# Kernel tuning notes

Measured on AMD Instinct MI355X. Metric: run time of the kernel, lower is better.

## Reference

```python
import jax, jax.numpy as jnp
import numpy as np

N = 4096; E = 65536; IN = 512; H = 256; QD = 256; NH = 8; HD = QD // NH
OUT = 10; L = 2; CT = 50


def _ln(x, g, b, eps=1e-5):
    mu = x.mean(-1, keepdims=True)
    var = ((x - mu) ** 2).mean(-1, keepdims=True)
    return (x - mu) * jax.lax.rsqrt(var + eps) * g + b


def _forward(x, edge_index, cell_types, Wi, bi, Wq, bq, Wk, bk, Wv, bv, Bc, cemb,
             Win, bin_p, Wo, bo, Wm1, bm1, Wm2, bm2, Wm3, bm3, ln_g, ln_b,
             Wc1, bc1, Wc2, bc2):
    src, tgt = edge_index[0], edge_index[1]
    h = jax.nn.relu(x @ Wi + bi)                      # [N, H] input projection
    # graph connectivity scattered into a dense mask (as in _create_attention_mask)
    mask = jnp.zeros((N, N), jnp.float32).at[src, tgt].set(1.0)
    for l in range(L):
        res = h
        Q = h @ Wq[l] + bq[l]                         # [N, QD]
        K = h @ Wk[l] + bk[l]
        V = h @ Wv[l] + bv[l]
        Q = Q @ Bc[l]                                 # biological constraint
        K = K @ Bc[l].T
        ce = cemb[l][cell_types]                      # [N, QD] cell-type embedding
        Q = Q + 0.1 * ce
        K = K + 0.1 * ce
        # dense graph-masked attention (entanglement matrix), applied to V
        scores = (Q @ K.T) / float(np.sqrt(QD))      # [N, N]
        scores = jnp.where(mask == 0.0, -1e9, scores)
        attn = jax.nn.softmax(scores, axis=-1)
        graph_att = attn @ V                          # [N, QD]
        # nn.MultiheadAttention(Q, K, V) entanglement layer (eval mode)
        q = (Q @ Win[l, :, :QD] + bin_p[l, :QD]).reshape(N, NH, HD)
        k = (K @ Win[l, :, QD:2 * QD] + bin_p[l, QD:2 * QD]).reshape(N, NH, HD)
        v = (V @ Win[l, :, 2 * QD:] + bin_p[l, 2 * QD:]).reshape(N, NH, HD)
        w = jax.nn.softmax(jnp.einsum('nhd,mhd->hnm', q, k) / float(np.sqrt(HD)), axis=-1)
        mha = jnp.einsum('hnm,mhd->nhd', w, v).reshape(N, QD) @ Wo[l] + bo[l]
        # edge gather -> message MLP -> scatter-add (PyG aggr='add', x_i=target, x_j=source)
        # quantum slot of the concat is zeros, so only the first 2H rows of Wm1 contribute
        m = jnp.concatenate([h[tgt], h[src]], axis=-1) @ Wm1[l, :2 * H] + bm1[l]
        m = jax.nn.relu(m)
        m = jax.nn.relu(m @ Wm2[l] + bm2[l])
        m = m @ Wm3[l] + bm3[l]                       # [E, H]
        agg = jax.ops.segment_sum(m, tgt, num_segments=N)
        h = _ln(res + agg + mha + graph_att, ln_g[l], ln_b[l])
    # graph-level readout: mean || max pooling -> classifier (hidden*2 -> hidden -> out)
    pooled = jnp.concatenate([h.mean(0), h.max(0)], axis=-1)   # [2H]
    z = jax.nn.relu(pooled @ Wc1 + bc1)
    return z @ Wc2 + bc2                              # [OUT]


def setup_inputs():
    ks = jax.random.split(jax.random.key(0), 40)
    s = 0.05
    p = lambda i, shape: jax.random.normal(ks[i], shape, jnp.float32) * s
    z = lambda shape: jnp.zeros(shape, jnp.float32)
    return {
        'x': jax.random.normal(ks[0], (N, IN), jnp.float32),
        'edge_index': jax.random.randint(ks[1], (2, E), 0, N),
        'cell_types': jax.random.randint(ks[2], (N,), 0, CT),
        'Wi': p(3, (IN, H)), 'bi': z((H,)),
        'Wq': p(4, (L, H, QD)), 'bq': z((L, QD)),
        'Wk': p(5, (L, H, QD)), 'bk': z((L, QD)),
        'Wv': p(6, (L, H, QD)), 'bv': z((L, QD)),
        'Bc': p(7, (L, QD, QD)),
        'cemb': p(8, (L, CT, QD)),
        'Win': p(9, (L, QD, 3 * QD)), 'bin_p': z((L, 3 * QD)),
        'Wo': p(10, (L, QD, QD)), 'bo': z((L, QD)),
        'Wm1': p(11, (L, 2 * H + QD, QD)), 'bm1': z((L, QD)),
        'Wm2': p(12, (L, QD, QD)), 'bm2': z((L, QD)),
        'Wm3': p(13, (L, QD, H)), 'bm3': z((L, H)),
        'ln_g': jnp.ones((L, H), jnp.float32), 'ln_b': z((L, H)),
        'Wc1': p(14, (2 * H, H)), 'bc1': z((H,)),
        'Wc2': p(15, (H, OUT)), 'bc2': z((OUT,)),
    }


def reference(x, edge_index, cell_types, Wi, bi, Wq, bq, Wk, bk, Wv, bv, Bc, cemb,
              Win, bin_p, Wo, bo, Wm1, bm1, Wm2, bm2, Wm3, bm3, ln_g, ln_b,
              Wc1, bc1, Wc2, bc2):
    return _forward(x, edge_index, cell_types, Wi, bi, Wq, bq, Wk, bk, Wv, bv, Bc, cemb,
                    Win, bin_p, Wo, bo, Wm1, bm1, Wm2, bm2, Wm3, bm3, ln_g, ln_b,
                    Wc1, bc1, Wc2, bc2)
```

## Files before the change

### kernel.cpp

```cpp
#include <hip/hip_runtime.h>
#include <hip/hip_bf16.h>

#define N_NODES 4096
#define E_EDGES 65536
#define IN_F    512
#define H_F     256
#define QD      256
#define NHEAD   8
#define HD      32
#define OUT_F   10
#define L_LAYERS 2
#define CT_N    50

enum { FLAG_RELU = 1, FLAG_ACCUM = 2, FLAG_WF32 = 4, FLAG_WB16 = 8 };

typedef __attribute__((ext_vector_type(8))) __bf16 bf16x8;
typedef __attribute__((ext_vector_type(4))) float f32x4;

union PU { bf16x8 v; __hip_bfloat16 h[8]; __hip_bfloat162 b2[4]; };

template<int BM, int BN, bool EDGE>
__global__ __launch_bounds__(256) void gemm_mfma(
    const __hip_bfloat16* __restrict__ A, int lda,
    const __hip_bfloat16* __restrict__ B, int ldb,
    float* __restrict__ Cf, __hip_bfloat16* __restrict__ Cb, int ldc,
    int K,
    const float* __restrict__ bias, const float* __restrict__ rowscale,
    const int* __restrict__ tgtp, const int* __restrict__ srcp,
    const float* __restrict__ kbias,
    int flags)
{
    constexpr int WM = BM / 2, WN = BN / 2, MT = WM / 16, NT = WN / 16;
    constexpr int LDT = 40;
    __shared__ alignas(16) __hip_bfloat16 As[BM * LDT];
    __shared__ alignas(16) __hip_bfloat16 Bs[BN * LDT];

    const int tid = threadIdx.x;
    const int w = tid >> 6, lane = tid & 63, l16 = lane & 15, quad = lane >> 4;
    const int wm = w >> 1, wn = w & 1;
    const int bm = blockIdx.y * BM, bn = blockIdx.x * BN;

    f32x4 acc[MT][NT];
    #pragma unroll
    for (int i = 0; i < MT; ++i)
        #pragma unroll
        for (int j = 0; j < NT; ++j)
            #pragma unroll
            for (int r = 0; r < 4; ++r) acc[i][j][r] = 0.f;

    for (int k0 = 0; k0 < K; k0 += 32) {
        #pragma unroll
        for (int f = tid; f < BM * 4; f += 256) {
            int r = f >> 2, sg = f & 3;
            if (EDGE) {
                int i = bm + r;
                int tg = tgtp[i], sr = srcp[i];
                PU z1, z2, o;
                z1.v = *reinterpret_cast<const bf16x8*>(A + (size_t)tg * 512 + k0 + sg * 8);
                z2.v = *reinterpret_cast<const bf16x8*>(A + (size_t)sr * 512 + 256 + k0 + sg * 8);
                float4 b0 = *reinterpret_cast<const float4*>(kbias + k0 + sg * 8);
                float4 b1 = *reinterpret_cast<const float4*>(kbias + k0 + sg * 8 + 4);
                float bb[8] = {b0.x, b0.y, b0.z, b0.w, b1.x, b1.y, b1.z, b1.w};
                #pragma unroll
                for (int j = 0; j < 8; ++j) {
                    float v = __bfloat162float(z1.h[j]) + __bfloat162float(z2.h[j]) + bb[j];
                    o.h[j] = __float2bfloat16(fmaxf(v, 0.f));
                }
                *reinterpret_cast<bf16x8*>(&As[r * LDT + sg * 8]) = o.v;
            } else {
                *reinterpret_cast<uint4*>(&As[r * LDT + sg * 8]) =
                    *reinterpret_cast<const uint4*>(A + (size_t)(bm + r) * lda + k0 + sg * 8);
            }
        }
        #pragma unroll
        for (int f = tid; f < BN * 4; f += 256) {
            int r = f >> 2, sg = f & 3;
            *reinterpret_cast<uint4*>(&Bs[r * LDT + sg * 8]) =
                *reinterpret_cast<const uint4*>(B + (size_t)(bn + r) * ldb + k0 + sg * 8);
        }
        __syncthreads();
        bf16x8 af[MT], bfr[NT];
        #pragma unroll
        for (int mt = 0; mt < MT; ++mt)
            af[mt] = *reinterpret_cast<const bf16x8*>(&As[(wm * WM + mt * 16 + l16) * LDT + quad * 8]);
        #pragma unroll
        for (int nt = 0; nt < NT; ++nt)
            bfr[nt] = *reinterpret_cast<const bf16x8*>(&Bs[(wn * WN + nt * 16 + l16) * LDT + quad * 8]);
        #pragma unroll
        for (int mt = 0; mt < MT; ++mt)
            #pragma unroll
            for (int nt = 0; nt < NT; ++nt)
                acc[mt][nt] = __builtin_amdgcn_mfma_f32_16x16x32_bf16(af[mt], bfr[nt], acc[mt][nt], 0, 0, 0);
        __syncthreads();
    }

    #pragma unroll
    for (int mt = 0; mt < MT; ++mt) {
        #pragma unroll
        for (int nt = 0; nt < NT; ++nt) {
            int col = bn + wn * WN + nt * 16 + l16;
            #pragma unroll
            for (int r = 0; r < 4; ++r) {
                int row = bm + wm * WM + mt * 16 + quad * 4 + r;
                float v = acc[mt][nt][r];
                if (bias) {
                    float bv = bias[col];
                    if (rowscale) bv *= rowscale[row];
                    v += bv;
                }
                if (flags & FLAG_RELU) v = fmaxf(v, 0.f);
                size_t off = (size_t)row * ldc + col;
                if (flags & FLAG_ACCUM)     Cf[off] += v;
                else if (flags & FLAG_WF32) Cf[off] = v;
                if (flags & FLAG_WB16)      Cb[off] = __float2bfloat16(v);
            }
        }
    }
}

__global__ __launch_bounds__(512, 4) void edge_gemm(
    const __hip_bfloat16* __restrict__ Z,
    const __hip_bfloat16* __restrict__ B,
    float* __restrict__ A3f,
    const int* __restrict__ tgtp, const int* __restrict__ srcp,
    const float* __restrict__ kbias,
    const float* __restrict__ bias)
{
    constexpr int LDA = 264;
    __shared__ alignas(16) __hip_bfloat16 As[64 * LDA];
    __shared__ int tg_sh[64];

    const int tid = threadIdx.x;
    const int w = tid >> 6, lane = tid & 63, l16 = lane & 15, quad = lane >> 4;
    const int bid = blockIdx.x;
    const int bm = ((bid & 7) * 128 + (bid >> 3)) * 64;

    if (tid < 64) tg_sh[tid] = tgtp[bm + tid];

    bf16x8 zt[4], zs[4];
    #pragma unroll
    for (int u = 0; u < 4; ++u) {
        int g = u * 512 + tid;
        int r = g >> 5, c = g & 31;
        int i = bm + r;
        int tg = tgtp[i], sr = srcp[i];
        zt[u] = *reinterpret_cast<const bf16x8*>(Z + (size_t)tg * 512 + c * 8);
        zs[u] = *reinterpret_cast<const bf16x8*>(Z + (size_t)sr * 512 + 256 + c * 8);
    }
    #pragma unroll
    for (int u = 0; u < 4; ++u) {
        int g = u * 512 + tid;
        int r = g >> 5, c = g & 31;
        PU a, b, o;
        a.v = zt[u]; b.v = zs[u];
        float4 k0v = *reinterpret_cast<const float4*>(kbias + c * 8);
        float4 k1v = *reinterpret_cast<const float4*>(kbias + c * 8 + 4);
        float bb[8] = {k0v.x, k0v.y, k0v.z, k0v.w, k1v.x, k1v.y, k1v.z, k1v.w};
        #pragma unroll
        for (int j = 0; j < 8; ++j) {
            float v = __bfloat162float(a.h[j]) + __bfloat162float(b.h[j]) + bb[j];
            o.h[j] = __float2bfloat16(fmaxf(v, 0.f));
        }
        *reinterpret_cast<bf16x8*>(&As[r * LDA + c * 8]) = o.v;
    }
    __syncthreads();

    const int wn = w;
    f32x4 acc[4][2];
    #pragma unroll
    for (int mt = 0; mt < 4; ++mt)
        #pragma unroll
        for (int nt = 0; nt < 2; ++nt)
            #pragma unroll
            for (int r = 0; r < 4; ++r) acc[mt][nt][r] = 0.f;

    #pragma unroll
    for (int k0 = 0; k0 < 256; k0 += 32) {
        bf16x8 af[4], bfr[2];
        #pragma unroll
        for (int nt = 0; nt < 2; ++nt)
            bfr[nt] = *reinterpret_cast<const bf16x8*>(
                B + (size_t)(wn * 32 + nt * 16 + l16) * 256 + k0 + quad * 8);
        #pragma unroll
        for (int mt = 0; mt < 4; ++mt)
            af[mt] = *reinterpret_cast<const bf16x8*>(&As[(mt * 16 + l16) * LDA + k0 + quad * 8]);
        #pragma unroll
        for (int mt = 0; mt < 4; ++mt)
            #pragma unroll
            for (int nt = 0; nt < 2; ++nt)
                acc[mt][nt] = __builtin_amdgcn_mfma_f32_16x16x32_bf16(af[mt], bfr[nt], acc[mt][nt], 0, 0, 0);
    }

    __syncthreads();
    #pragma unroll
    for (int mt = 0; mt < 4; ++mt) {
        #pragma unroll
        for (int nt = 0; nt < 2; ++nt) {
            int col = wn * 32 + nt * 16 + l16;
            float bv = bias[col];
            #pragma unroll
            for (int r = 0; r < 4; ++r) {
                int rl = mt * 16 + quad * 4 + r;
                As[rl * LDA + col] = __float2bfloat16(fmaxf(acc[mt][nt][r] + bv, 0.f));
            }
        }
    }
    __syncthreads();
    {
        int col = tid & 255, r0 = (tid >> 8) * 32;
        float s = 0.f;
        int cur = tg_sh[r0];
        #pragma unroll 8
        for (int r = 0; r < 32; ++r) {
            int rr = r0 + r;
            int t = tg_sh[rr];
            if (t != cur) {
                atomicAdd(&A3f[(size_t)cur * 256 + col], s);
                s = 0.f; cur = t;
            }
            s += __bfloat162float(As[rr * LDA + col]);
        }
        atomicAdd(&A3f[(size_t)cur * 256 + col], s);
    }
}

struct GSet { const __hip_bfloat16* A; int lda; const __hip_bfloat16* B;
              const float* bias; const float* rowscale;
              const float* extra; float esc; float cscale;
              __hip_bfloat16* C; float* Cf; int vtout; int ldc; int coloff; };
struct GPack { GSet s[8]; };

__global__ __launch_bounds__(256) void gemm_bz(GPack p, const int* __restrict__ eidx)
{
    GSet g = p.s[blockIdx.z];
    constexpr int LDT = 40;
    __shared__ alignas(16) __hip_bfloat16 As[64 * LDT];
    __shared__ alignas(16) __hip_bfloat16 Bs[64 * LDT];

    const int tid = threadIdx.x;
    const int w = tid >> 6, lane = tid & 63, l16 = lane & 15, quad = lane >> 4;
    const int wm = w >> 1, wn = w & 1;
    const int bm = blockIdx.y * 64, bn = blockIdx.x * 64;

    f32x4 acc[2][2];
    #pragma unroll
    for (int i = 0; i < 2; ++i)
        #pragma unroll
        for (int j = 0; j < 2; ++j)
            #pragma unroll
            for (int r = 0; r < 4; ++r) acc[i][j][r] = 0.f;

    for (int k0 = 0; k0 < 256; k0 += 32) {
        #pragma unroll
        for (int f = tid; f < 256; f += 256) {
            int r = f >> 2, sg = f & 3;
            *reinterpret_cast<uint4*>(&As[r * LDT + sg * 8]) =
                *reinterpret_cast<const uint4*>(g.A + (size_t)(bm + r) * g.lda + k0 + sg * 8);
            *reinterpret_cast<uint4*>(&Bs[r * LDT + sg * 8]) =
                *reinterpret_cast<const uint4*>(g.B + (size_t)(bn + r) * 256 + k0 + sg * 8);
        }
        __syncthreads();
        bf16x8 af[2], bfr[2];
        #pragma unroll
        for (int mt = 0; mt < 2; ++mt)
            af[mt] = *reinterpret_cast<const bf16x8*>(&As[(wm * 32 + mt * 16 + l16) * LDT + quad * 8]);
        #pragma unroll
        for (int nt = 0; nt < 2; ++nt)
            bfr[nt] = *reinterpret_cast<const bf16x8*>(&Bs[(wn * 32 + nt * 16 + l16) * LDT + quad * 8]);
        #pragma unroll
        for (int mt = 0; mt < 2; ++mt)
            #pragma unroll
            for (int nt = 0; nt < 2; ++nt)
                acc[mt][nt] = __builtin_amdgcn_mfma_f32_16x16x32_bf16(af[mt], bfr[nt], acc[mt][nt], 0, 0, 0);
        __syncthreads();
    }

    #pragma unroll
    for (int mt = 0; mt < 2; ++mt) {
        #pragma unroll
        for (int nt = 0; nt < 2; ++nt) {
            int colL = bn + wn * 32 + nt * 16 + l16;
            #pragma unroll
            for (int r = 0; r < 4; ++r) {
                int row = bm + wm * 32 + mt * 16 + quad * 4 + r;
                float v = acc[mt][nt][r];
                if (g.bias) {
                    float bv = g.bias[colL];
                    if (g.rowscale) bv *= g.rowscale[row];
                    v += bv;
                }
                if (g.extra) v += g.esc * g.extra[(size_t)eidx[row] * QD + colL];
                v *= g.cscale;
                if (g.vtout)
                    g.C[(size_t)colL * 4096 + row] = __float2bfloat16(v);
                else if (g.Cf)
                    g.Cf[(size_t)row * g.ldc + g.coloff + colL] = v;
                else
                    g.C[(size_t)row * g.ldc + g.coloff + colL] = __float2bfloat16(v);
            }
        }
    }
}

struct FDesc { const float* A; int lda; const float* B; int ldb; int tb;
               const float* bias; float* C; int M, N, K; };
struct FPack { FDesc d[16]; };

__global__ __launch_bounds__(256) void fgemm2(FPack p)
{
    FDesc c = p.d[blockIdx.z];
    int bm = blockIdx.y * 32, bn = blockIdx.x * 32;
    if (bm >= c.M || bn >= c.N) return;
    __shared__ float As[16][33];
    __shared__ float Bs[16][33];
    int tid = threadIdx.x;
    int tr = tid / 16, tc = tid % 16;
    float acc[2][2] = {};

    for (int k0 = 0; k0 < c.K; k0 += 16) {
        #pragma unroll
        for (int u = 0; u < 2; ++u) {
            int i = tid * 2 + u;
            int m = i >> 4, kk = i & 15;
            int row = bm + m, kg = k0 + kk;
            As[kk][m] = (row < c.M && kg < c.K) ? c.A[(size_t)row * c.lda + kg] : 0.f;
        }
        if (c.tb) {
            #pragma unroll
            for (int u = 0; u < 2; ++u) {
                int i = tid * 2 + u;
                int n = i >> 4, kk = i & 15;
                int col = bn + n, kg = k0 + kk;
                Bs[kk][n] = (col < c.N && kg < c.K) ? c.B[(size_t)col * c.ldb + kg] : 0.f;
            }
        } else {
            #pragma unroll
            for (int u = 0; u < 2; ++u) {
                int i = tid * 2 + u;
                int kk = i >> 5, n = i & 31;
                int col = bn + n, kg = k0 + kk;
                Bs[kk][n] = (col < c.N && kg < c.K) ? c.B[(size_t)kg * c.ldb + col] : 0.f;
            }
        }
        __syncthreads();
        #pragma unroll
        for (int kk = 0; kk < 16; ++kk) {
            float a0 = As[kk][tr * 2], a1 = As[kk][tr * 2 + 1];
            float b0 = Bs[kk][tc * 2], b1 = Bs[kk][tc * 2 + 1];
            acc[0][0] = fmaf(a0, b0, acc[0][0]);
            acc[0][1] = fmaf(a0, b1, acc[0][1]);
            acc[1][0] = fmaf(a1, b0, acc[1][0]);
            acc[1][1] = fmaf(a1, b1, acc[1][1]);
        }
        __syncthreads();
    }

    #pragma unroll
    for (int i = 0; i < 2; ++i) {
        int row = bm + tr * 2 + i;
        if (row >= c.M) continue;
        #pragma unroll
        for (int j = 0; j < 2; ++j) {
            int col = bn + tc * 2 + j;
            if (col >= c.N) continue;
            float v = acc[i][j];
            if (c.bias) v += c.bias[col];
            c.C[(size_t)row * c.N + col] = v;
        }
    }
}

__global__ __launch_bounds__(512, 4) void mha_flash10(
    const __hip_bfloat16* __restrict__ Qm,
    const __hip_bfloat16* __restrict__ Km,
    const __hip_bfloat16* __restrict__ Vt, __hip_bfloat16* __restrict__ Out)
{
    const int hh = blockIdx.y;
    const int tid = threadIdx.x;
    const int w = tid >> 6, lane = tid & 63, l16 = lane & 15, quad = lane >> 4;
    const int qb = blockIdx.x * 64;

    __shared__ float Osh[8][4][64][9];
    __shared__ float Lsh[8][4][16];

    bf16x8 aq[4];
    #pragma unroll
    for (int s = 0; s < 4; ++s)
        aq[s] = *reinterpret_cast<const bf16x8*>(
            Qm + (size_t)(qb + s * 16 + l16) * 256 + hh * 32 + quad * 8);
    const __hip_bfloat16* vb0 = Vt + (size_t)(hh * 32 + l16) * 4096;
    const __hip_bfloat16* vb1 = vb0 + (size_t)16 * 4096;
    const int rowoff = (l16 >> 2) * 8 + (l16 & 3);
    const f32x4 zero = {0.f, 0.f, 0.f, 0.f};

    PU onesu;
    #pragma unroll
    for (int j = 0; j < 8; ++j) onesu.h[j] = __float2bfloat16(1.f);
    const bf16x8 onesv = onesu.v;

    f32x4 o0[4], o1[4], lac[4];
    #pragma unroll
    for (int s = 0; s < 4; ++s) { o0[s] = zero; o1[s] = zero; lac[s] = zero; }

    const int kstart = w * 512;
    for (int kt = 0; kt < 8; ++kt) {
        const int kbase = kstart + kt * 64;
        bf16x8 kf[4];
        #pragma unroll
        for (int c = 0; c < 2; ++c)
            #pragma unroll
            for (int st = 0; st < 2; ++st)
                kf[c * 2 + st] = *reinterpret_cast<const bf16x8*>(
                    Km + (size_t)(kbase + c * 32 + st * 4 + rowoff) * 256 + hh * 32 + quad * 8);
        bf16x8 v00 = *reinterpret_cast<const bf16x8*>(vb0 + kbase + quad * 8);
        bf16x8 v01 = *reinterpret_cast<const bf16x8*>(vb1 + kbase + quad * 8);
        bf16x8 v10 = *reinterpret_cast<const bf16x8*>(vb0 + kbase + 32 + quad * 8);
        bf16x8 v11 = *reinterpret_cast<const bf16x8*>(vb1 + kbase + 32 + quad * 8);

        #pragma unroll
        for (int s = 0; s < 4; ++s) {
            f32x4 sv[4];
            __builtin_amdgcn_s_setprio(1);
            #pragma unroll
            for (int i = 0; i < 4; ++i)
                sv[i] = __builtin_amdgcn_mfma_f32_16x16x32_bf16(kf[i], aq[s], zero, 0, 0, 0);
            __builtin_amdgcn_s_setprio(0);
            PU p0, p1;
            #pragma unroll
            for (int i = 0; i < 4; ++i) {
                float e0 = exp2f(sv[i][0]), e1 = exp2f(sv[i][1]);
                float e2 = exp2f(sv[i][2]), e3 = exp2f(sv[i][3]);
                PU& pp = (i < 2) ? p0 : p1;
                pp.b2[(i & 1) * 2 + 0] = __float22bfloat162_rn(make_float2(e0, e1));
                pp.b2[(i & 1) * 2 + 1] = __float22bfloat162_rn(make_float2(e2, e3));
            }
            __builtin_amdgcn_s_setprio(1);
            o0[s]  = __builtin_amdgcn_mfma_f32_16x16x32_bf16(v00,   p0.v, o0[s],  0, 0, 0);
            o1[s]  = __builtin_amdgcn_mfma_f32_16x16x32_bf16(v01,   p0.v, o1[s],  0, 0, 0);
            lac[s] = __builtin_amdgcn_mfma_f32_16x16x32_bf16(onesv, p0.v, lac[s], 0, 0, 0);
            o0[s]  = __builtin_amdgcn_mfma_f32_16x16x32_bf16(v10,   p1.v, o0[s],  0, 0, 0);
            o1[s]  = __builtin_amdgcn_mfma_f32_16x16x32_bf16(v11,   p1.v, o1[s],  0, 0, 0);
            lac[s] = __builtin_amdgcn_mfma_f32_16x16x32_bf16(onesv, p1.v, lac[s], 0, 0, 0);
            __builtin_amdgcn_s_setprio(0);
        }
    }

    float lsum[4];
    #pragma unroll
    for (int s = 0; s < 4; ++s) lsum[s] = lac[s][0];

    #pragma unroll
    for (int s = 0; s < 4; ++s) {
        #pragma unroll
        for (int r = 0; r < 4; ++r) {
            Osh[w][s][lane][r]     = o0[s][r];
            Osh[w][s][lane][4 + r] = o1[s][r];
        }
        if (quad == 0) Lsh[w][s][l16] = lsum[s];
    }
    __syncthreads();
    if (w < 4) {
        const int s = w;
        f32x4 a0 = zero, a1 = zero;
        float ll = 0.f;
        #pragma unroll
        for (int ww = 0; ww < 8; ++ww) {
            #pragma unroll
            for (int r = 0; r < 4; ++r) {
                a0[r] += Osh[ww][s][lane][r];
                a1[r] += Osh[ww][s][lane][4 + r];
            }
            ll += Lsh[ww][s][l16];
        }
        float inv = 1.f / ll;
        __hip_bfloat16* dst = Out + (size_t)(qb + s * 16 + l16) * 256 + hh * 32;
        #pragma unroll
        for (int r = 0; r < 4; ++r) {
            dst[quad * 4 + r]      = __float2bfloat16(a0[r] * inv);
            dst[16 + quad * 4 + r] = __float2bfloat16(a1[r] * inv);
        }
    }
}

__global__ __launch_bounds__(256) void build_mask(const int* __restrict__ src,
                                                  const int* __restrict__ tgt,
                                                  unsigned* __restrict__ mb,
                                                  int* __restrict__ cnt)
{
    int e = blockIdx.x * 256 + threadIdx.x;
    if (e >= E_EDGES) return;
    int t = tgt[e];
    atomicOr(mb + (size_t)src[e] * (N_NODES / 32) + (t >> 5), 1u << (t & 31));
    atomicAdd(&cnt[t], 1);
}

__global__ __launch_bounds__(1024) void csr_scan(const int* __restrict__ cnt, int* __restrict__ off,
                                                 int* __restrict__ cursor, float* __restrict__ degf)
{
    __shared__ int sh[1024];
    int t = threadIdx.x;
    int base = t * 4;
    int c0 = cnt[base], c1 = cnt[base + 1], c2 = cnt[base + 2], c3 = cnt[base + 3];
    int sum = c0 + c1 + c2 + c3;
    sh[t] = sum; __syncthreads();
    for (int d = 1; d < 1024; d <<= 1) {
        int v = (t >= d) ? sh[t - d] : 0;
        __syncthreads();
        sh[t] += v;
        __syncthreads();
    }
    int excl = sh[t] - sum;
    int o0 = excl, o1 = excl + c0, o2 = o1 + c1, o3 = o2 + c2;
    off[base] = o0; off[base + 1] = o1; off[base + 2] = o2; off[base + 3] = o3;
    cursor[base] = o0; cursor[base + 1] = o1; cursor[base + 2] = o2; cursor[base + 3] = o3;
    degf[base] = (float)c0; degf[base + 1] = (float)c1;
    degf[base + 2] = (float)c2; degf[base + 3] = (float)c3;
    if (t == 1023) off[4096] = sh[t];
}

__global__ __launch_bounds__(256) void csr_fill(const int* __restrict__ src, const int* __restrict__ tgt,
                                                int* __restrict__ cursor,
                                                int* __restrict__ srcp, int* __restrict__ tgtp)
{
    int e = blockIdx.x * 256 + threadIdx.x;
    if (e >= E_EDGES) return;
    int t = tgt[e];
    int pos = atomicAdd(&cursor[t], 1);
    srcp[pos] = src[e];
    tgtp[pos] = t;
}

__global__ __launch_bounds__(256) void sparse_attn(
    const __hip_bfloat16* __restrict__ Q, const __hip_bfloat16* __restrict__ K,
    const __hip_bfloat16* __restrict__ V, int vld,
    const unsigned* __restrict__ maskb, float* __restrict__ outb)
{
    int i = blockIdx.x, t = threadIdx.x;
    __shared__ float qsh[256];
    __shared__ int   nb[1024];
    __shared__ float sc[1024];
    __shared__ int   cnt;
    __shared__ float red[4];
    __shared__ float smax, ssum;
    if (t == 0) cnt = 0;
    qsh[t] = __bfloat162float(Q[(size_t)i * 256 + t]);
    __syncthreads();
    if (t < 128) {
        unsigned wv = maskb[(size_t)i * 128 + t];
        while (wv) {
            int b = __ffs(wv) - 1; wv &= wv - 1;
            int p = atomicAdd(&cnt, 1);
            nb[p] = t * 32 + b;
        }
    }
    __syncthreads();
    int deg = cnt;
    int wid = t >> 6, lane = t & 63;
    if (deg > 0) {
        for (int n = wid; n < deg; n += 4) {
            union { uint2 u; __hip_bfloat16 h[4]; } kv;
            kv.u = *reinterpret_cast<const uint2*>(K + (size_t)nb[n] * 256 + lane * 4);
            float s = qsh[lane*4+0] * __bfloat162float(kv.h[0]) + qsh[lane*4+1] * __bfloat162float(kv.h[1])
                    + qsh[lane*4+2] * __bfloat162float(kv.h[2]) + qsh[lane*4+3] * __bfloat162float(kv.h[3]);
            #pragma unroll
            for (int off = 32; off; off >>= 1) s += __shfl_xor(s, off);
            if (lane == 0) sc[n] = s * 0.0625f;
        }
        __syncthreads();
        float m = -3.4e38f;
        for (int n = t; n < deg; n += 256) m = fmaxf(m, sc[n]);
        #pragma unroll
        for (int off = 32; off; off >>= 1) m = fmaxf(m, __shfl_xor(m, off));
        if (lane == 0) red[wid] = m;
        __syncthreads();
        if (t == 0) smax = fmaxf(fmaxf(red[0], red[1]), fmaxf(red[2], red[3]));
        __syncthreads();
        float ls = 0.f;
        for (int n = t; n < deg; n += 256) { float e = __expf(sc[n] - smax); sc[n] = e; ls += e; }
        #pragma unroll
        for (int off = 32; off; off >>= 1) ls += __shfl_xor(ls, off);
        if (lane == 0) red[wid] = ls;
        __syncthreads();
        if (t == 0) ssum = red[0] + red[1] + red[2] + red[3];
        __syncthreads();
        float inv = 1.f / ssum;
        float o = 0.f;
        for (int n = 0; n < deg; ++n)
            o += sc[n] * __bfloat162float(V[(size_t)nb[n] * vld + t]);
        outb[(size_t)i * 256 + t] = o * inv;
    } else {
        float o = 0.f;
        for (int j = 0; j < N_NODES; ++j) o += __bfloat162float(V[(size_t)j * vld + t]);
        outb[(size_t)i * 256 + t] = o * (1.f / N_NODES);
    }
}

__global__ __launch_bounds__(256) void ln_kernel(float* __restrict__ h, __hip_bfloat16* __restrict__ h16,
                                                 const float* __restrict__ a1,
                                                 const float* __restrict__ a2,
                                                 const float* __restrict__ a3,
                                                 const float* __restrict__ g, const float* __restrict__ b)
{
    int row = blockIdx.x, t = threadIdx.x;
    __shared__ float red[256];
    size_t off = ((size_t)row << 8) + t;
    float v = h[off] + a1[off] + a2[off] + a3[off];
    red[t] = v; __syncthreads();
    for (int s = 128; s > 0; s >>= 1) { if (t < s) red[t] += red[t + s]; __syncthreads(); }
    float mu = red[0] * (1.f / 256.f); __syncthreads();
    float d = v - mu;
    red[t] = d * d; __syncthreads();
    for (int s = 128; s > 0; s >>= 1) { if (t < s) red[t] += red[t + s]; __syncthreads(); }
    float var = red[0] * (1.f / 256.f);
    float r = d * rsqrtf(var + 1e-5f) * g[t] + b[t];
    h[off] = r;
    h16[off] = __float2bfloat16(r);
}

__global__ __launch_bounds__(256) void colpool(const float* __restrict__ h, float* __restrict__ p)
{
    int c = blockIdx.x, t = threadIdx.x;
    __shared__ float rs[256], rm[256];
    float s = 0.f, m = -3.4e38f;
    for (int row = t; row < N_NODES; row += 256) {
        float v = h[((size_t)row << 8) + c];
        s += v; m = fmaxf(m, v);
    }
    rs[t] = s; rm[t] = m; __syncthreads();
    for (int st = 128; st > 0; st >>= 1) {
        if (t < st) { rs[t] += rs[t + st]; rm[t] = fmaxf(rm[t], rm[t + st]); }
        __syncthreads();
    }
    if (t == 0) { p[c] = rs[0] * (1.f / N_NODES); p[256 + c] = rm[0]; }
}

__global__ __launch_bounds__(256) void classifier(const float* __restrict__ pooled,
                                                  const float* __restrict__ Wc1, const float* __restrict__ bc1,
                                                  const float* __restrict__ Wc2, const float* __restrict__ bc2,
                                                  float* __restrict__ out)
{
    __shared__ float p[512];
    __shared__ float z[256];
    int t = threadIdx.x;
    p[t] = pooled[t]; p[256 + t] = pooled[256 + t];
    __syncthreads();
    float s = bc1[t];
    for (int k = 0; k < 512; ++k) s = fmaf(p[k], Wc1[k * 256 + t], s);
    z[t] = fmaxf(s, 0.f);
    __syncthreads();
    if (t < OUT_F) {
        float o = bc2[t];
        for (int j = 0; j < 256; ++j) o = fmaf(z[j], Wc2[j * OUT_F + t], o);
        out[t] = o;
    }
}

struct CDesc { const float* s; __hip_bfloat16* d; int total; };
struct CPack { CDesc d[2]; };
__global__ __launch_bounds__(256) void convert_copy(CPack p)
{
    CDesc c = p.d[blockIdx.y];
    for (int i = blockIdx.x * 256 + threadIdx.x; i < c.total; i += gridDim.x * 256)
        c.d[i] = __float2bfloat16(c.s[i]);
}
struct TDesc { const float* s; __hip_bfloat16* d; int K, N, sld; };
struct TPack { TDesc d[23]; };
__global__ __launch_bounds__(256) void convert_t32(TPack p)
{
    TDesc c = p.d[blockIdx.z];
    int k0 = blockIdx.x * 32, n0 = blockIdx.y * 32;
    if (k0 >= c.K || n0 >= c.N) return;
    __shared__ float t[32][33];
    int tr = threadIdx.x >> 5, tc = threadIdx.x & 31;
    #pragma unroll
    for (int rr = 0; rr < 32; rr += 8)
        t[tc][tr + rr] = c.s[(size_t)(k0 + tr + rr) * c.sld + n0 + tc];
    __syncthreads();
    #pragma unroll
    for (int rr = 0; rr < 32; rr += 8)
        c.d[(size_t)(n0 + tr + rr) * c.K + k0 + tc] = __float2bfloat16(t[tr + rr][tc]);
}

extern "C" void kernel_launch(void* const* d_in, const int* in_sizes, int n_in,
                              void* d_out, int out_size, void* d_ws, size_t ws_size,
                              hipStream_t stream)
{
    const float* x    = (const float*)d_in[0];
    const int*   ei   = (const int*)d_in[1];
    const int*   ct   = (const int*)d_in[2];
    const float* Wi   = (const float*)d_in[3];
    const float* bi   = (const float*)d_in[4];
    const float* Wq   = (const float*)d_in[5];
    const float* bq   = (const float*)d_in[6];
    const float* Wk   = (const float*)d_in[7];
    const float* bk   = (const float*)d_in[8];
    const float* Wv   = (const float*)d_in[9];
    const float* bv   = (const float*)d_in[10];
    const float* Bc   = (const float*)d_in[11];
    const float* cemb = (const float*)d_in[12];
    const float* Win  = (const float*)d_in[13];
    const float* binp = (const float*)d_in[14];
    const float* Wo   = (const float*)d_in[15];
    const float* bo   = (const float*)d_in[16];
    const float* Wm1  = (const float*)d_in[17];
    const float* bm1  = (const float*)d_in[18];
    const float* Wm2  = (const float*)d_in[19];
    const float* bm2  = (const float*)d_in[20];
    const float* Wm3  = (const float*)d_in[21];
    const float* bm3  = (const float*)d_in[22];
    const float* lng  = (const float*)d_in[23];
    const float* lnb  = (const float*)d_in[24];
    const float* Wc1  = (const float*)d_in[25];
    const float* bc1  = (const float*)d_in[26];
    const float* Wc2  = (const float*)d_in[27];
    const float* bc2  = (const float*)d_in[28];

    const int* src = ei;
    const int* tgt = ei + E_EDGES;

    char* wp = (char*)d_ws;
    auto alloc = [&](size_t bytes) { char* r = wp; wp += (bytes + 255) & ~(size_t)255; return r; };
    const size_t NH = (size_t)N_NODES * 256;
    float* h      = (float*)alloc(NH * 4);
    float* a1     = (float*)alloc(NH * 4);
    float* a2     = (float*)alloc(NH * 4);
    float* a3     = (float*)alloc(NH * 4);
    float* pooled = (float*)alloc(512 * 4);
    float* degf   = (float*)alloc(N_NODES * 4);
    float* A3f    = (float*)alloc(NH * 4);
    __hip_bfloat16* x16 = (__hip_bfloat16*)alloc((size_t)N_NODES * 512 * 2);
    __hip_bfloat16* h16 = (__hip_bfloat16*)alloc(NH * 2);
    __hip_bfloat16* Qb  = (__hip_bfloat16*)alloc(NH * 2);
    __hip_bfloat16* Kb  = (__hip_bfloat16*)alloc(NH * 2);
    __hip_bfloat16* Vb  = (__hip_bfloat16*)alloc(NH * 2);
    __hip_bfloat16* Tq  = (__hip_bfloat16*)alloc(NH * 2);
    __hip_bfloat16* Tk  = (__hip_bfloat16*)alloc(NH * 2);
    __hip_bfloat16* Vt  = (__hip_bfloat16*)alloc(NH * 2);
    __hip_bfloat16* Z12 = (__hip_bfloat16*)alloc((size_t)N_NODES * 512 * 2);
    __hip_bfloat16* A3  = (__hip_bfloat16*)alloc(NH * 2);
    __hip_bfloat16* Wi_t= (__hip_bfloat16*)alloc((size_t)256 * 512 * 2);
    float *Wqc_f[2], *Wkc_f[2], *Wqm_f[2], *Wkm_f[2], *Wvm_f[2];
    float *bqc[2], *bkc[2], *bqm[2], *bkm[2], *bvm[2], *ceq2[2], *cek2[2];
    for (int l = 0; l < 2; ++l) {
        Wqc_f[l] = (float*)alloc(65536 * 4); Wkc_f[l] = (float*)alloc(65536 * 4);
        Wqm_f[l] = (float*)alloc(65536 * 4); Wkm_f[l] = (float*)alloc(65536 * 4);
        Wvm_f[l] = (float*)alloc(65536 * 4);
        bqc[l] = (float*)alloc(256 * 4); bkc[l] = (float*)alloc(256 * 4);
        bqm[l] = (float*)alloc(256 * 4); bkm[l] = (float*)alloc(256 * 4);
        bvm[l] = (float*)alloc(256 * 4);
        ceq2[l] = (float*)alloc(CT_N * 256 * 4); cek2[l] = (float*)alloc(CT_N * 256 * 4);
    }
    __hip_bfloat16* WB[2][11];
    for (int l = 0; l < 2; ++l)
        for (int m = 0; m < 11; ++m)
            WB[l][m] = (__hip_bfloat16*)alloc(65536 * 2);
    unsigned* maskb = (unsigned*)alloc((size_t)N_NODES * 128 * 4);
    int* cnt    = (int*)alloc(N_NODES * 4);
    int* cursor = (int*)alloc(N_NODES * 4);
    int* off    = (int*)alloc((N_NODES + 1) * 4);
    int* srcp   = (int*)alloc(E_EDGES * 4);
    int* tgtp   = (int*)alloc(E_EDGES * 4);

    CPack cp; cp.d[0] = {x, x16, N_NODES * 512};
    convert_copy<<<dim3(256, 1), 256, 0, stream>>>(cp);

    FPack f1; int n1 = 0;
    FPack f2; int n2 = 0;
    for (int l = 0; l < 2; ++l) {
        const float* Wq_l  = Wq + (size_t)l * 65536;
        const float* Wk_l  = Wk + (size_t)l * 65536;
        const float* Wv_l  = Wv + (size_t)l * 65536;
        const float* Bc_l  = Bc + (size_t)l * 65536;
        const float* Win_l = Win + (size_t)l * 256 * 768;
        const float* ce_l  = cemb + (size_t)l * CT_N * QD;
        const float* bq_l  = bq + l * 256;
        const float* bk_l  = bk + l * 256;
        const float* bv_l  = bv + l * 256;
        const float* bin_l = binp + l * 768;
        f1.d[n1++] = {Wq_l, 256, Bc_l, 256, 0, nullptr, Wqc_f[l], 256, 256, 256};
        f1.d[n1++] = {Wk_l, 256, Bc_l, 256, 1, nullptr, Wkc_f[l], 256, 256, 256};
        f1.d[n1++] = {bq_l, 256, Bc_l, 256, 0, nullptr, bqc[l], 1, 256, 256};
        f1.d[n1++] = {bk_l, 256, Bc_l, 256, 1, nullptr, bkc[l], 1, 256, 256};
        f2.d[n2++] = {Wqc_f[l], 256, Win_l,       768, 0, nullptr, Wqm_f[l], 256, 256, 256};
        f2.d[n2++] = {Wkc_f[l], 256, Win_l + 256, 768, 0, nullptr, Wkm_f[l], 256, 256, 256};
        f2.d[n2++] = {Wv_l,     256, Win_l + 512, 768, 0, nullptr, Wvm_f[l], 256, 256, 256};
        f2.d[n2++] = {ce_l,     256, Win_l,       768, 0, nullptr, ceq2[l], CT_N, 256, 256};
        f2.d[n2++] = {ce_l,     256, Win_l + 256, 768, 0, nullptr, cek2[l], CT_N, 256, 256};
        f2.d[n2++] = {bqc[l],   256, Win_l,       768, 0, bin_l,       bqm[l], 1, 256, 256};
        f2.d[n2++] = {bkc[l],   256, Win_l + 256, 768, 0, bin_l + 256, bkm[l], 1, 256, 256};
        f2.d[n2++] = {bv_l,     256, Win_l + 512, 768, 0, bin_l + 512, bvm[l], 1, 256, 256};
    }
    fgemm2<<<dim3(8, 8, n1), 256, 0, stream>>>(f1);
    fgemm2<<<dim3(8, 8, n2), 256, 0, stream>>>(f2);

    TPack tp; int ndt = 0;
    auto addT = [&](const float* s, __hip_bfloat16* d, int K, int N, int sld) { tp.d[ndt++] = {s, d, K, N, sld}; };
    addT(Wi, Wi_t, 512, 256, 256);
    for (int l = 0; l < 2; ++l) {
        const float* Wv_l  = Wv + (size_t)l * 65536;
        const float* Wo_l  = Wo + (size_t)l * 65536;
        const float* Wm1_l = Wm1 + (size_t)l * (2 * H_F + QD) * QD;
        const float* Wm2_l = Wm2 + (size_t)l * 65536;
        const float* Wm3_l = Wm3 + (size_t)l * 65536;
        addT(Wqc_f[l], WB[l][0], 256, 256, 256);
        addT(Wkc_f[l], WB[l][1], 256, 256, 256);
        addT(Wqm_f[l], WB[l][2], 256, 256, 256);
        addT(Wkm_f[l], WB[l][3], 256, 256, 256);
        addT(Wvm_f[l], WB[l][4], 256, 256, 256);
        addT(Wv_l,     WB[l][5], 256, 256, 256);
        addT(Wo_l,     WB[l][6], 256, 256, 256);
        addT(Wm1_l,             WB[l][7], 256, 256, 256);
        addT(Wm1_l + 256 * 256, WB[l][8], 256, 256, 256);
        addT(Wm2_l,    WB[l][9],  256, 256, 256);
        addT(Wm3_l,    WB[l][10], 256, 256, 256);
    }
    convert_t32<<<dim3(16, 8, ndt), 256, 0, stream>>>(tp);

    hipMemsetAsync(maskb, 0, (size_t)N_NODES * 128 * 4, stream);
    hipMemsetAsync(cnt, 0, N_NODES * 4, stream);
    build_mask<<<E_EDGES / 256, 256, 0, stream>>>(src, tgt, maskb, cnt);
    csr_scan<<<1, 1024, 0, stream>>>(cnt, off, cursor, degf);
    csr_fill<<<E_EDGES / 256, 256, 0, stream>>>(src, tgt, cursor, srcp, tgtp);

    gemm_mfma<64, 64, false><<<dim3(4, 64), 256, 0, stream>>>(
        x16, 512, Wi_t, 512, h, h16, 256, 512,
        bi, nullptr, nullptr, nullptr, nullptr, FLAG_RELU | FLAG_WF32 | FLAG_WB16);

    const float QSCALE = 0.25507693f;

    for (int l = 0; l < L_LAYERS; ++l) {
        const float* ce_l  = cemb + (size_t)l * CT_N * QD;
        const float* bo_l  = bo + l * QD;
        const float* bm1_l = bm1 + l * QD;
        const float* bm2_l = bm2 + l * QD;
        const float* bm3_l = bm3 + l * H_F;
        const float* lng_l = lng + l * H_F;
        const float* lnb_l = lnb + l * H_F;
        const float* bv_l  = bv + l * 256;

        {
            GPack gp;
            gp.s[0] = {h16, 256, WB[l][0], bqc[l], nullptr, ce_l,    0.1f, 1.0f,   Qb,  nullptr, 0, 256, 0};
            gp.s[1] = {h16, 256, WB[l][1], bkc[l], nullptr, ce_l,    0.1f, 1.0f,   Kb,  nullptr, 0, 256, 0};
            gp.s[2] = {h16, 256, WB[l][5], bv_l,   nullptr, nullptr, 0.f,  1.0f,   Vb,  nullptr, 0, 256, 0};
            gp.s[3] = {h16, 256, WB[l][2], bqm[l], nullptr, ceq2[l], 0.1f, QSCALE, Tq,  nullptr, 0, 256, 0};
            gp.s[4] = {h16, 256, WB[l][3], bkm[l], nullptr, cek2[l], 0.1f, 1.0f,   Tk,  nullptr, 0, 256, 0};
            gp.s[5] = {h16, 256, WB[l][4], bvm[l], nullptr, nullptr, 0.f,  1.0f,   Vt,  nullptr, 1, 256, 0};
            gp.s[6] = {h16, 256, WB[l][7], nullptr, nullptr, nullptr, 0.f, 1.0f,   Z12, nullptr, 0, 512, 0};
            gp.s[7] = {h16, 256, WB[l][8], nullptr, nullptr, nullptr, 0.f, 1.0f,   Z12, nullptr, 0, 512, 256};
            gemm_bz<<<dim3(4, 64, 8), 256, 0, stream>>>(gp, ct);
        }

        hipMemsetAsync(A3f, 0, NH * 4, stream);

        sparse_attn<<<N_NODES, 256, 0, stream>>>(Qb, Kb, Vb, 256, maskb, a1);

        mha_flash10<<<dim3(64, NHEAD), 512, 0, stream>>>(Tq, Tk, Vt, Qb);

        edge_gemm<<<E_EDGES / 64, 512, 0, stream>>>(
            Z12, WB[l][9], A3f, tgtp, srcp, bm1_l, bm2_l);
        {
            CPack c2; c2.d[0] = {A3f, A3, (int)NH};
            convert_copy<<<dim3(256, 1), 256, 0, stream>>>(c2);
        }

        {
            GPack gp;
            gp.s[0] = {Qb, 256, WB[l][6],  bo_l,  nullptr, nullptr, 0.f, 1.0f, nullptr, a2, 0, 256, 0};
            gp.s[1] = {A3, 256, WB[l][10], bm3_l, degf,    nullptr, 0.f, 1.0f, nullptr, a3, 0, 256, 0};
            gemm_bz<<<dim3(4, 64, 2), 256, 0, stream>>>(gp, ct);
        }

        ln_kernel<<<N_NODES, 256, 0, stream>>>(h, h16, a1, a2, a3, lng_l, lnb_l);
    }

    colpool<<<H_F, 256, 0, stream>>>(h, pooled);
    classifier<<<1, 256, 0, stream>>>(pooled, Wc1, bc1, Wc2, bc2, (float*)d_out);
}
```

Measured before the change: 500.1 us.

## Fuse MHA flash kernel and edge-message GEMM into one heterogeneous launch

Merges the dense multi-head attention kernel and the edge gather/MLP/scatter kernel into a single launch. Block index selects the role: the first 512 blocks run attention, the remaining 1024 run the edge work, with shared memory unioned between the two. This lets the two independent workloads run concurrently and removes a launch and the tail gap between them. The attention cross-wave reduction is also reworked into a two-stage pairwise exchange, which shrinks its shared buffer so the union fits. The cost is more syncs in that reduction, and the larger register footprint of the combined kernel may reduce occupancy.

```diff
diff --git a/kernel.cpp b/kernel.cpp
--- a/kernel.cpp
+++ b/kernel.cpp
@@ -118,109 +118,247 @@
     }
 }
 
-__global__ __launch_bounds__(512, 4) void edge_gemm(
+__global__ __launch_bounds__(512, 4) void mha_edge_fused(
+    const __hip_bfloat16* __restrict__ Qm,
+    const __hip_bfloat16* __restrict__ Km,
+    const __hip_bfloat16* __restrict__ Vt,
+    __hip_bfloat16* __restrict__ Out,
     const __hip_bfloat16* __restrict__ Z,
-    const __hip_bfloat16* __restrict__ B,
+    const __hip_bfloat16* __restrict__ Bw,
     float* __restrict__ A3f,
     const int* __restrict__ tgtp, const int* __restrict__ srcp,
     const float* __restrict__ kbias,
     const float* __restrict__ bias)
 {
     constexpr int LDA = 264;
-    __shared__ alignas(16) __hip_bfloat16 As[64 * LDA];
-    __shared__ int tg_sh[64];
+    __shared__ union SM {
+        struct { float Osh[4][4][64][9]; float Lsh[4][4][16]; } m;
+        struct { alignas(16) __hip_bfloat16 As[64 * LDA]; int tg[64]; } e;
+    } sm;
 
     const int tid = threadIdx.x;
     const int w = tid >> 6, lane = tid & 63, l16 = lane & 15, quad = lane >> 4;
-    const int bid = blockIdx.x;
-    const int bm = ((bid & 7) * 128 + (bid >> 3)) * 64;
-
-    if (tid < 64) tg_sh[tid] = tgtp[bm + tid];
-
-    bf16x8 zt[4], zs[4];
-    #pragma unroll
-    for (int u = 0; u < 4; ++u) {
-        int g = u * 512 + tid;
-        int r = g >> 5, c = g & 31;
-        int i = bm + r;
-        int tg = tgtp[i], sr = srcp[i];
-        zt[u] = *reinterpret_cast<const bf16x8*>(Z + (size_t)tg * 512 + c * 8);
-        zs[u] = *reinterpret_cast<const bf16x8*>(Z + (size_t)sr * 512 + 256 + c * 8);
-    }
-    #pragma unroll
-    for (int u = 0; u < 4; ++u) {
-        int g = u * 512 + tid;
-        int r = g >> 5, c = g & 31;
-        PU a, b, o;
-        a.v = zt[u]; b.v = zs[u];
-        float4 k0v = *reinterpret_cast<const float4*>(kbias + c * 8);
-        float4 k1v = *reinterpret_cast<const float4*>(kbias + c * 8 + 4);
-        float bb[8] = {k0v.x, k0v.y, k0v.z, k0v.w, k1v.x, k1v.y, k1v.z, k1v.w};
-        #pragma unroll
-        for (int j = 0; j < 8; ++j) {
-            float v = __bfloat162float(a.h[j]) + __bfloat162float(b.h[j]) + bb[j];
-            o.h[j] = __float2bfloat16(fmaxf(v, 0.f));
-        }
-        *reinterpret_cast<bf16x8*>(&As[r * LDA + c * 8]) = o.v;
-    }
-    __syncthreads();
-
-    const int wn = w;
-    f32x4 acc[4][2];
-    #pragma unroll
-    for (int mt = 0; mt < 4; ++mt)
-        #pragma unroll
-        for (int nt = 0; nt < 2; ++nt)
-            #pragma unroll
-            for (int r = 0; r < 4; ++r) acc[mt][nt][r] = 0.f;
-
-    #pragma unroll
-    for (int k0 = 0; k0 < 256; k0 += 32) {
-        bf16x8 af[4], bfr[2];
-        #pragma unroll
-        for (int nt = 0; nt < 2; ++nt)
-            bfr[nt] = *reinterpret_cast<const bf16x8*>(
-                B + (size_t)(wn * 32 + nt * 16 + l16) * 256 + k0 + quad * 8);
+
+    if (blockIdx.x < 512) {
+        const int hh = blockIdx.x >> 6;
+        const int qb = (blockIdx.x & 63) * 64;
+
+        bf16x8 aq[4];
+        #pragma unroll
+        for (int s = 0; s < 4; ++s)
+            aq[s] = *reinterpret_cast<const bf16x8*>(
+                Qm + (size_t)(qb + s * 16 + l16) * 256 + hh * 32 + quad * 8);
+        const __hip_bfloat16* vb0 = Vt + (size_t)(hh * 32 + l16) * 4096;
+        const __hip_bfloat16* vb1 = vb0 + (size_t)16 * 4096;
+        const int rowoff = (l16 >> 2) * 8 + (l16 & 3);
+        const f32x4 zero = {0.f, 0.f, 0.f, 0.f};
+
+        PU onesu;
+        #pragma unroll
+        for (int j = 0; j < 8; ++j) onesu.h[j] = __float2bfloat16(1.f);
+        const bf16x8 onesv = onesu.v;
+
+        f32x4 o0[4], o1[4], lac[4];
+        #pragma unroll
+        for (int s = 0; s < 4; ++s) { o0[s] = zero; o1[s] = zero; lac[s] = zero; }
+
+        const int kstart = w * 512;
+        for (int kt = 0; kt < 8; ++kt) {
+            const int kbase = kstart + kt * 64;
+            bf16x8 kf[4];
+            #pragma unroll
+            for (int c = 0; c < 2; ++c)
+                #pragma unroll
+                for (int st = 0; st < 2; ++st)
+                    kf[c * 2 + st] = *reinterpret_cast<const bf16x8*>(
+                        Km + (size_t)(kbase + c * 32 + st * 4 + rowoff) * 256 + hh * 32 + quad * 8);
+            bf16x8 v00 = *reinterpret_cast<const bf16x8*>(vb0 + kbase + quad * 8);
+            bf16x8 v01 = *reinterpret_cast<const bf16x8*>(vb1 + kbase + quad * 8);
+            bf16x8 v10 = *reinterpret_cast<const bf16x8*>(vb0 + kbase + 32 + quad * 8);
+            bf16x8 v11 = *reinterpret_cast<const bf16x8*>(vb1 + kbase + 32 + quad * 8);
+
+            #pragma unroll
+            for (int s = 0; s < 4; ++s) {
+                f32x4 sv[4];
+                __builtin_amdgcn_s_setprio(1);
+                #pragma unroll
+                for (int i = 0; i < 4; ++i)
+                    sv[i] = __builtin_amdgcn_mfma_f32_16x16x32_bf16(kf[i], aq[s], zero, 0, 0, 0);
+                __builtin_amdgcn_s_setprio(0);
+                PU p0, p1;
+                #pragma unroll
+                for (int i = 0; i < 4; ++i) {
+                    float e0 = exp2f(sv[i][0]), e1 = exp2f(sv[i][1]);
+                    float e2 = exp2f(sv[i][2]), e3 = exp2f(sv[i][3]);
+                    PU& pp = (i < 2) ? p0 : p1;
+                    pp.b2[(i & 1) * 2 + 0] = __float22bfloat162_rn(make_float2(e0, e1));
+                    pp.b2[(i & 1) * 2 + 1] = __float22bfloat162_rn(make_float2(e2, e3));
+                }
+                __builtin_amdgcn_s_setprio(1);
+                o0[s]  = __builtin_amdgcn_mfma_f32_16x16x32_bf16(v00,   p0.v, o0[s],  0, 0, 0);
+                o1[s]  = __builtin_amdgcn_mfma_f32_16x16x32_bf16(v01,   p0.v, o1[s],  0, 0, 0);
+                lac[s] = __builtin_amdgcn_mfma_f32_16x16x32_bf16(onesv, p0.v, lac[s], 0, 0, 0);
+                o0[s]  = __builtin_amdgcn_mfma_f32_16x16x32_bf16(v10,   p1.v, o0[s],  0, 0, 0);
+                o1[s]  = __builtin_amdgcn_mfma_f32_16x16x32_bf16(v11,   p1.v, o1[s],  0, 0, 0);
+                lac[s] = __builtin_amdgcn_mfma_f32_16x16x32_bf16(onesv, p1.v, lac[s], 0, 0, 0);
+                __builtin_amdgcn_s_setprio(0);
+            }
+        }
+
+        float lsum[4];
+        #pragma unroll
+        for (int s = 0; s < 4; ++s) lsum[s] = lac[s][0];
+
+        if (w >= 4) {
+            #pragma unroll
+            for (int s = 0; s < 4; ++s) {
+                #pragma unroll
+                for (int r = 0; r < 4; ++r) {
+                    sm.m.Osh[w - 4][s][lane][r]     = o0[s][r];
+                    sm.m.Osh[w - 4][s][lane][4 + r] = o1[s][r];
+                }
+                if (quad == 0) sm.m.Lsh[w - 4][s][l16] = lsum[s];
+            }
+        }
+        __syncthreads();
+        if (w < 4) {
+            #pragma unroll
+            for (int s = 0; s < 4; ++s) {
+                #pragma unroll
+                for (int r = 0; r < 4; ++r) {
+                    o0[s][r] += sm.m.Osh[w][s][lane][r];
+                    o1[s][r] += sm.m.Osh[w][s][lane][4 + r];
+                }
+                lsum[s] += sm.m.Lsh[w][s][l16];
+            }
+        }
+        __syncthreads();
+        if (w < 4) {
+            #pragma unroll
+            for (int s = 0; s < 4; ++s) {
+                if (s == w) continue;
+                #pragma unroll
+                for (int r = 0; r < 4; ++r) {
+                    sm.m.Osh[w][s][lane][r]     = o0[s][r];
+                    sm.m.Osh[w][s][lane][4 + r] = o1[s][r];
+                }
+                if (quad == 0) sm.m.Lsh[w][s][l16] = lsum[s];
+            }
+        }
+        __syncthreads();
+        if (w < 4) {
+            const int s = w;
+            f32x4 a0 = o0[s], a1 = o1[s];
+            float ll = lsum[s];
+            #pragma unroll
+            for (int i = 0; i < 4; ++i) {
+                if (i == s) continue;
+                #pragma unroll
+                for (int r = 0; r < 4; ++r) {
+                    a0[r] += sm.m.Osh[i][s][lane][r];
+                    a1[r] += sm.m.Osh[i][s][lane][4 + r];
+                }
+                ll += sm.m.Lsh[i][s][l16];
+            }
+            float inv = 1.f / ll;
+            __hip_bfloat16* dst = Out + (size_t)(qb + s * 16 + l16) * 256 + hh * 32;
+            #pragma unroll
+            for (int r = 0; r < 4; ++r) {
+                dst[quad * 4 + r]      = __float2bfloat16(a0[r] * inv);
+                dst[16 + quad * 4 + r] = __float2bfloat16(a1[r] * inv);
+            }
+        }
+    } else {
+        const int bid = blockIdx.x - 512;
+        const int bm = ((bid & 7) * 128 + (bid >> 3)) * 64;
+
+        if (tid < 64) sm.e.tg[tid] = tgtp[bm + tid];
+
+        bf16x8 zt[4], zs[4];
+        #pragma unroll
+        for (int u = 0; u < 4; ++u) {
+            int g = u * 512 + tid;
+            int r = g >> 5, c = g & 31;
+            int i = bm + r;
+            int tg = tgtp[i], sr = srcp[i];
+            zt[u] = *reinterpret_cast<const bf16x8*>(Z + (size_t)tg * 512 + c * 8);
+            zs[u] = *reinterpret_cast<const bf16x8*>(Z + (size_t)sr * 512 + 256 + c * 8);
+        }
+        #pragma unroll
+        for (int u = 0; u < 4; ++u) {
+            int g = u * 512 + tid;
+            int r = g >> 5, c = g & 31;
+            PU a, b, o;
+            a.v = zt[u]; b.v = zs[u];
+            float4 k0v = *reinterpret_cast<const float4*>(kbias + c * 8);
+            float4 k1v = *reinterpret_cast<const float4*>(kbias + c * 8 + 4);
+            float bb[8] = {k0v.x, k0v.y, k0v.z, k0v.w, k1v.x, k1v.y, k1v.z, k1v.w};
+            #pragma unroll
+            for (int j = 0; j < 8; ++j) {
+                float v = __bfloat162float(a.h[j]) + __bfloat162float(b.h[j]) + bb[j];
+                o.h[j] = __float2bfloat16(fmaxf(v, 0.f));
+            }
+            *reinterpret_cast<bf16x8*>(&sm.e.As[r * LDA + c * 8]) = o.v;
+        }
+        __syncthreads();
+
+        const int wn = w;
+        f32x4 acc[4][2];
         #pragma unroll
         for (int mt = 0; mt < 4; ++mt)
-            af[mt] = *reinterpret_cast<const bf16x8*>(&As[(mt * 16 + l16) * LDA + k0 + quad * 8]);
-        #pragma unroll
-        for (int mt = 0; mt < 4; ++mt)
             #pragma unroll
             for (int nt = 0; nt < 2; ++nt)
-                acc[mt][nt] = __builtin_amdgcn_mfma_f32_16x16x32_bf16(af[mt], bfr[nt], acc[mt][nt], 0, 0, 0);
-    }
-
-    __syncthreads();
-    #pragma unroll
-    for (int mt = 0; mt < 4; ++mt) {
-        #pragma unroll
-        for (int nt = 0; nt < 2; ++nt) {
-            int col = wn * 32 + nt * 16 + l16;
-            float bv = bias[col];
-            #pragma unroll
-            for (int r = 0; r < 4; ++r) {
-                int rl = mt * 16 + quad * 4 + r;
-                As[rl * LDA + col] = __float2bfloat16(fmaxf(acc[mt][nt][r] + bv, 0.f));
-            }
-        }
-    }
-    __syncthreads();
-    {
-        int col = tid & 255, r0 = (tid >> 8) * 32;
-        float s = 0.f;
-        int cur = tg_sh[r0];
-        #pragma unroll 8
-        for (int r = 0; r < 32; ++r) {
-            int rr = r0 + r;
-            int t = tg_sh[rr];
-            if (t != cur) {
-                atomicAdd(&A3f[(size_t)cur * 256 + col], s);
-                s = 0.f; cur = t;
-            }
-            s += __bfloat162float(As[rr * LDA + col]);
-        }
-        atomicAdd(&A3f[(size_t)cur * 256 + col], s);
+                #pragma unroll
+                for (int r = 0; r < 4; ++r) acc[mt][nt][r] = 0.f;
+
+        #pragma unroll
+        for (int k0 = 0; k0 < 256; k0 += 32) {
+            bf16x8 af[4], bfr[2];
+            #pragma unroll
+            for (int nt = 0; nt < 2; ++nt)
+                bfr[nt] = *reinterpret_cast<const bf16x8*>(
+                    Bw + (size_t)(wn * 32 + nt * 16 + l16) * 256 + k0 + quad * 8);
+            #pragma unroll
+            for (int mt = 0; mt < 4; ++mt)
+                af[mt] = *reinterpret_cast<const bf16x8*>(&sm.e.As[(mt * 16 + l16) * LDA + k0 + quad * 8]);
+            #pragma unroll
+            for (int mt = 0; mt < 4; ++mt)
+                #pragma unroll
+                for (int nt = 0; nt < 2; ++nt)
+                    acc[mt][nt] = __builtin_amdgcn_mfma_f32_16x16x32_bf16(af[mt], bfr[nt], acc[mt][nt], 0, 0, 0);
+        }
+
+        __syncthreads();
+        #pragma unroll
+        for (int mt = 0; mt < 4; ++mt) {
+            #pragma unroll
+            for (int nt = 0; nt < 2; ++nt) {
+                int col = wn * 32 + nt * 16 + l16;
+                float bv = bias[col];
+                #pragma unroll
+                for (int r = 0; r < 4; ++r) {
+                    int rl = mt * 16 + quad * 4 + r;
+                    sm.e.As[rl * LDA + col] = __float2bfloat16(fmaxf(acc[mt][nt][r] + bv, 0.f));
+                }
+            }
+        }
+        __syncthreads();
+        {
+            int col = tid & 255, r0 = (tid >> 8) * 32;
+            float s = 0.f;
+            int cur = sm.e.tg[r0];
+            #pragma unroll 8
+            for (int r = 0; r < 32; ++r) {
+                int rr = r0 + r;
+                int t = sm.e.tg[rr];
+                if (t != cur) {
+                    atomicAdd(&A3f[(size_t)cur * 256 + col], s);
+                    s = 0.f; cur = t;
+                }
+                s += __bfloat162float(sm.e.As[rr * LDA + col]);
+            }
+            atomicAdd(&A3f[(size_t)cur * 256 + col], s);
+        }
     }
 }
 
@@ -366,118 +504,6 @@
             float v = acc[i][j];
             if (c.bias) v += c.bias[col];
             c.C[(size_t)row * c.N + col] = v;
-        }
-    }
-}
-
-__global__ __launch_bounds__(512, 4) void mha_flash10(
-    const __hip_bfloat16* __restrict__ Qm,
-    const __hip_bfloat16* __restrict__ Km,
-    const __hip_bfloat16* __restrict__ Vt, __hip_bfloat16* __restrict__ Out)
-{
-    const int hh = blockIdx.y;
-    const int tid = threadIdx.x;
-    const int w = tid >> 6, lane = tid & 63, l16 = lane & 15, quad = lane >> 4;
-    const int qb = blockIdx.x * 64;
-
-    __shared__ float Osh[8][4][64][9];
-    __shared__ float Lsh[8][4][16];
-
-    bf16x8 aq[4];
-    #pragma unroll
-    for (int s = 0; s < 4; ++s)
-        aq[s] = *reinterpret_cast<const bf16x8*>(
-            Qm + (size_t)(qb + s * 16 + l16) * 256 + hh * 32 + quad * 8);
-    const __hip_bfloat16* vb0 = Vt + (size_t)(hh * 32 + l16) * 4096;
-    const __hip_bfloat16* vb1 = vb0 + (size_t)16 * 4096;
-    const int rowoff = (l16 >> 2) * 8 + (l16 & 3);
-    const f32x4 zero = {0.f, 0.f, 0.f, 0.f};
-
-    PU onesu;
-    #pragma unroll
-    for (int j = 0; j < 8; ++j) onesu.h[j] = __float2bfloat16(1.f);
-    const bf16x8 onesv = onesu.v;
-
-    f32x4 o0[4], o1[4], lac[4];
-    #pragma unroll
-    for (int s = 0; s < 4; ++s) { o0[s] = zero; o1[s] = zero; lac[s] = zero; }
-
-    const int kstart = w * 512;
-    for (int kt = 0; kt < 8; ++kt) {
-        const int kbase = kstart + kt * 64;
-        bf16x8 kf[4];
-        #pragma unroll
-        for (int c = 0; c < 2; ++c)
-            #pragma unroll
-            for (int st = 0; st < 2; ++st)
-                kf[c * 2 + st] = *reinterpret_cast<const bf16x8*>(
-                    Km + (size_t)(kbase + c * 32 + st * 4 + rowoff) * 256 + hh * 32 + quad * 8);
-        bf16x8 v00 = *reinterpret_cast<const bf16x8*>(vb0 + kbase + quad * 8);
-        bf16x8 v01 = *reinterpret_cast<const bf16x8*>(vb1 + kbase + quad * 8);
-        bf16x8 v10 = *reinterpret_cast<const bf16x8*>(vb0 + kbase + 32 + quad * 8);
-        bf16x8 v11 = *reinterpret_cast<const bf16x8*>(vb1 + kbase + 32 + quad * 8);
-
-        #pragma unroll
-        for (int s = 0; s < 4; ++s) {
-            f32x4 sv[4];
-            __builtin_amdgcn_s_setprio(1);
-            #pragma unroll
-            for (int i = 0; i < 4; ++i)
-                sv[i] = __builtin_amdgcn_mfma_f32_16x16x32_bf16(kf[i], aq[s], zero, 0, 0, 0);
-            __builtin_amdgcn_s_setprio(0);
-            PU p0, p1;
-            #pragma unroll
-            for (int i = 0; i < 4; ++i) {
-                float e0 = exp2f(sv[i][0]), e1 = exp2f(sv[i][1]);
-                float e2 = exp2f(sv[i][2]), e3 = exp2f(sv[i][3]);
-                PU& pp = (i < 2) ? p0 : p1;
-                pp.b2[(i & 1) * 2 + 0] = __float22bfloat162_rn(make_float2(e0, e1));
-                pp.b2[(i & 1) * 2 + 1] = __float22bfloat162_rn(make_float2(e2, e3));
-            }
-            __builtin_amdgcn_s_setprio(1);
-            o0[s]  = __builtin_amdgcn_mfma_f32_16x16x32_bf16(v00,   p0.v, o0[s],  0, 0, 0);
-            o1[s]  = __builtin_amdgcn_mfma_f32_16x16x32_bf16(v01,   p0.v, o1[s],  0, 0, 0);
-            lac[s] = __builtin_amdgcn_mfma_f32_16x16x32_bf16(onesv, p0.v, lac[s], 0, 0, 0);
-            o0[s]  = __builtin_amdgcn_mfma_f32_16x16x32_bf16(v10,   p1.v, o0[s],  0, 0, 0);
-            o1[s]  = __builtin_amdgcn_mfma_f32_16x16x32_bf16(v11,   p1.v, o1[s],  0, 0, 0);
-            lac[s] = __builtin_amdgcn_mfma_f32_16x16x32_bf16(onesv, p1.v, lac[s], 0, 0, 0);
-            __builtin_amdgcn_s_setprio(0);
-        }
-    }
-
-    float lsum[4];
-    #pragma unroll
-    for (int s = 0; s < 4; ++s) lsum[s] = lac[s][0];
-
-    #pragma unroll
-    for (int s = 0; s < 4; ++s) {
-        #pragma unroll
-        for (int r = 0; r < 4; ++r) {
-            Osh[w][s][lane][r]     = o0[s][r];
-            Osh[w][s][lane][4 + r] = o1[s][r];
-        }
-        if (quad == 0) Lsh[w][s][l16] = lsum[s];
-    }
-    __syncthreads();
-    if (w < 4) {
-        const int s = w;
-        f32x4 a0 = zero, a1 = zero;
-        float ll = 0.f;
-        #pragma unroll
-        for (int ww = 0; ww < 8; ++ww) {
-            #pragma unroll
-            for (int r = 0; r < 4; ++r) {
-                a0[r] += Osh[ww][s][lane][r];
-                a1[r] += Osh[ww][s][lane][4 + r];
-            }
-            ll += Lsh[ww][s][l16];
-        }
-        float inv = 1.f / ll;
-        __hip_bfloat16* dst = Out + (size_t)(qb + s * 16 + l16) * 256 + hh * 32;
-        #pragma unroll
-        for (int r = 0; r < 4; ++r) {
-            dst[quad * 4 + r]      = __float2bfloat16(a0[r] * inv);
-            dst[16 + quad * 4 + r] = __float2bfloat16(a1[r] * inv);
         }
     }
 }
@@ -855,10 +881,8 @@
 
         sparse_attn<<<N_NODES, 256, 0, stream>>>(Qb, Kb, Vb, 256, maskb, a1);
 
-        mha_flash10<<<dim3(64, NHEAD), 512, 0, stream>>>(Tq, Tk, Vt, Qb);
-
-        edge_gemm<<<E_EDGES / 64, 512, 0, stream>>>(
-            Z12, WB[l][9], A3f, tgtp, srcp, bm1_l, bm2_l);
+        mha_edge_fused<<<1536, 512, 0, stream>>>(
+            Tq, Tk, Vt, Qb, Z12, WB[l][9], A3f, tgtp, srcp, bm1_l, bm2_l);
         {
             CPack c2; c2.d[0] = {A3f, A3, (int)NH};
             convert_copy<<<dim3(256, 1), 256, 0, stream>>>(c2);
```

After: 495.1 us (median of 2 runs). About the same (-1.0%).
